# Kernel optimization log

Hardware: AMD Instinct MI355X
Metric: run time of the kernel (lower is better)

## Reference

```python
import jax, jax.numpy as jnp
import numpy as np

IN_FEATURES = 4096
OUT_FEATURES = 4096
N_TOKENS = 1024

@jax.custom_vjp
def binarize(w):
    # UnipolarSte.forward: (w > 0).float()
    return (w > 0).astype(w.dtype)

def _bin_fwd(w):
    return binarize(w), None

def _bin_bwd(_, g):
    # UnipolarSte.backward: F.hardtanh(grad_output) == clip(g, -1, 1)
    return (jnp.clip(g, -1.0, 1.0),)

binarize.defvjp(_bin_fwd, _bin_bwd)

def setup_inputs() -> dict:
    key = jax.random.key(0)
    kx, kw = jax.random.split(key)
    x = jax.random.normal(kx, (N_TOKENS, IN_FEATURES), dtype=jnp.float32)
    weight = jax.random.normal(kw, (OUT_FEATURES, IN_FEATURES), dtype=jnp.float32)
    scaling_factor = jnp.ones((OUT_FEATURES,), dtype=jnp.float32)
    return {"x": x, "weight": weight, "scaling_factor": scaling_factor}

def reference(x, weight, scaling_factor):
    w_b = binarize(weight)                      # [out, in] in {0,1}
    out = jnp.einsum('ni,oi->no', x, w_b)       # F.linear(x, w_b)
    # s_eff = round(clamp(s,1)).detach() - s.detach() + s
    s_round = jax.lax.stop_gradient(jnp.round(jnp.clip(scaling_factor, 1.0, None)))
    s_eff = s_round - jax.lax.stop_gradient(scaling_factor) + scaling_factor
    return out * s_eff[None, :]
```

## Files before the change

### kernel.cpp

```cpp
#include <hip/hip_runtime.h>

#define M_TOK 1024
#define NOUT  4096
#define KIN   4096
#define KBYTES (KIN / 8)

#define BM 128
#define BN 128
#define BK 64
#define NKT (KIN / BK)

typedef __attribute__((ext_vector_type(8))) short bf16x8_t;
typedef __attribute__((ext_vector_type(4))) float f32x4_t;

__global__ __launch_bounds__(256) void prep_w(const float* __restrict__ w,
                                              unsigned long long* __restrict__ wbits) {
  const int lane = threadIdx.x & 63;
  const int row  = blockIdx.x * 4 + (threadIdx.x >> 6);
  const float* wr = w + (size_t)row * KIN;
  unsigned long long mine = 0;
#pragma unroll 16
  for (int q = 0; q < 64; ++q) {
    float v = wr[q * 64 + lane];
    unsigned long long m = __ballot(v > 0.f);
    if (lane == q) mine = m;
  }
  wbits[(size_t)row * 64 + lane] = mine;
}

__device__ __forceinline__ unsigned pack_bf16(float a, float b) {
  unsigned ua = __float_as_uint(a);
  unsigned ub = __float_as_uint(b);
  ua = (ua + 0x7FFFu + ((ua >> 16) & 1u)) >> 16;
  ub = (ub + 0x7FFFu + ((ub >> 16) & 1u)) >> 16;
  return ua | (ub << 16);
}

__global__ __launch_bounds__(256) void prep_x(const float4* __restrict__ x4,
                                              uint2* __restrict__ xb) {
  const size_t t = blockIdx.x * 256 + threadIdx.x;
  float4 v = x4[t];
  xb[t] = make_uint2(pack_bf16(v.x, v.y), pack_bf16(v.z, v.w));
}

__global__ __launch_bounds__(512, 2) void gemm_bin_kernel(
    const unsigned short* __restrict__ A,
    const unsigned char* __restrict__ Wb,
    const float* __restrict__ sf,
    float* __restrict__ C) {
  __shared__ __align__(16) unsigned short As[2][BM * BK];
  __shared__ __align__(16) unsigned short Bs[2][BN * BK];

  const int tid  = threadIdx.x;
  const int lane = tid & 63;
  const int wave = tid >> 6;
  const int wm   = (wave >> 2) * 64;
  const int wn   = (wave & 3) * 32;
  const int quad = lane >> 4;
  const int l16  = lane & 15;
  const int m0   = blockIdx.y * BM;
  const int n0   = blockIdx.x * BN;

  const int r  = tid >> 2;
  const int j2 = tid & 3;
  const unsigned short* gA = A + (size_t)(m0 + r) * KIN + j2 * 16;
  const unsigned char*  gB = Wb + (size_t)(n0 + r) * KBYTES + j2 * 2;
  const int cw0 = ((2 * j2 + 0 + r) & 7);
  const int cw1 = ((2 * j2 + 1 + r) & 7);
  const int woA0 = r * BK + cw0 * 8, woA1 = r * BK + cw1 * 8;

  f32x4_t acc[4][2];
#pragma unroll
  for (int i = 0; i < 4; ++i)
#pragma unroll
    for (int j = 0; j < 2; ++j)
      acc[i][j] = (f32x4_t){0.f, 0.f, 0.f, 0.f};

  uint4 sa0 = *(const uint4*)gA;
  uint4 sa1 = *(const uint4*)(gA + 8);
  unsigned short sb = *(const unsigned short*)gB;

  for (int kt = 0; kt < NKT; ++kt) {
    const int cur = kt & 1;
    uint4 bx0, bx1;
    bx0.x = (sb & 0x1u    ? 0x3F80u : 0u) | (sb & 0x2u    ? 0x3F800000u : 0u);
    bx0.y = (sb & 0x4u    ? 0x3F80u : 0u) | (sb & 0x8u    ? 0x3F800000u : 0u);
    bx0.z = (sb & 0x10u   ? 0x3F80u : 0u) | (sb & 0x20u   ? 0x3F800000u : 0u);
    bx0.w = (sb & 0x40u   ? 0x3F80u : 0u) | (sb & 0x80u   ? 0x3F800000u : 0u);
    bx1.x = (sb & 0x100u  ? 0x3F80u : 0u) | (sb & 0x200u  ? 0x3F800000u : 0u);
    bx1.y = (sb & 0x400u  ? 0x3F80u : 0u) | (sb & 0x800u  ? 0x3F800000u : 0u);
    bx1.z = (sb & 0x1000u ? 0x3F80u : 0u) | (sb & 0x2000u ? 0x3F800000u : 0u);
    bx1.w = (sb & 0x4000u ? 0x3F80u : 0u) | (sb & 0x8000u ? 0x3F800000u : 0u);
    *(uint4*)&As[cur][woA0] = sa0;
    *(uint4*)&As[cur][woA1] = sa1;
    *(uint4*)&Bs[cur][woA0] = bx0;
    *(uint4*)&Bs[cur][woA1] = bx1;
    __syncthreads();
    if (kt + 1 < NKT) {
      const int off = (kt + 1) * BK;
      sa0 = *(const uint4*)(gA + off);
      sa1 = *(const uint4*)(gA + off + 8);
      sb  = *(const unsigned short*)(gB + (kt + 1) * 8);
    }
    bf16x8_t af[2][4], bfr[2][2];
#pragma unroll
    for (int ks = 0; ks < 2; ++ks) {
#pragma unroll
      for (int i = 0; i < 4; ++i) {
        const int ra = wm + i * 16 + l16;
        af[ks][i] = *(const bf16x8_t*)&As[cur][ra * BK + ((ks * 4 + quad + ra) & 7) * 8];
      }
#pragma unroll
      for (int j = 0; j < 2; ++j) {
        const int rb = wn + j * 16 + l16;
        bfr[ks][j] = *(const bf16x8_t*)&Bs[cur][rb * BK + ((ks * 4 + quad + rb) & 7) * 8];
      }
    }
#pragma unroll
    for (int ks = 0; ks < 2; ++ks)
#pragma unroll
      for (int i = 0; i < 4; ++i)
#pragma unroll
        for (int j = 0; j < 2; ++j)
          acc[i][j] = __builtin_amdgcn_mfma_f32_16x16x32_bf16(af[ks][i], bfr[ks][j],
                                                              acc[i][j], 0, 0, 0);
  }

#pragma unroll
  for (int j = 0; j < 2; ++j) {
    const int n = n0 + wn + j * 16 + l16;
    const float s = rintf(fmaxf(sf[n], 1.0f));
#pragma unroll
    for (int i = 0; i < 4; ++i) {
      const int mr = m0 + wm + i * 16 + quad * 4;
#pragma unroll
      for (int rr = 0; rr < 4; ++rr)
        C[(size_t)(mr + rr) * NOUT + n] = acc[i][j][rr] * s;
    }
  }
}

extern "C" void kernel_launch(void* const* d_in, const int* in_sizes, int n_in,
                              void* d_out, int out_size, void* d_ws, size_t ws_size,
                              hipStream_t stream) {
  const float* x  = (const float*)d_in[0];
  const float* w  = (const float*)d_in[1];
  const float* sf = (const float*)d_in[2];
  float* out = (float*)d_out;

  unsigned char*  Wbits = (unsigned char*)d_ws;
  unsigned short* Xb    = (unsigned short*)((char*)d_ws + (1u << 21));

  prep_w<<<1024, 256, 0, stream>>>(w, (unsigned long long*)Wbits);
  prep_x<<<4096, 256, 0, stream>>>((const float4*)x, (uint2*)Xb);

  dim3 grid(NOUT / BN, M_TOK / BM);
  gemm_bin_kernel<<<grid, 512, 0, stream>>>(Xb, Wbits, sf, out);
}
```

Baseline: 171.7 us.

## Prepack X and weight bits into MFMA fragment order and drop LDS staging

Adds a second weight prep pass that reorders the bit-packed weights into per-lane MFMA fragment order, and makes the X prep write bf16 directly in fragment layout. The GEMM then loads operands straight from global memory into registers with a two-stage register double buffer. This removes shared memory, barriers and the LDS round trip. Tiles become 128x64 per block with 4 waves. The cost is an extra prep launch, and each wave rereads A fragments from global/L2 with no LDS sharing across waves.

```diff
diff --git a/kernel.cpp b/kernel.cpp
--- a/kernel.cpp
+++ b/kernel.cpp
@@ -3,15 +3,10 @@
 #define M_TOK 1024
 #define NOUT  4096
 #define KIN   4096
-#define KBYTES (KIN / 8)
-
-#define BM 128
-#define BN 128
-#define BK 64
-#define NKT (KIN / BK)
 
 typedef __attribute__((ext_vector_type(8))) short bf16x8_t;
 typedef __attribute__((ext_vector_type(4))) float f32x4_t;
+
 
 __global__ __launch_bounds__(256) void prep_w(const float* __restrict__ w,
                                               unsigned long long* __restrict__ wbits) {
@@ -28,6 +23,17 @@
   wbits[(size_t)row * 64 + lane] = mine;
 }
 
+__global__ __launch_bounds__(256) void prep_w2(const unsigned long long* __restrict__ wbits,
+                                               unsigned short* __restrict__ bfrag) {
+  const unsigned t = blockIdx.x * 256 + threadIdx.x;
+  const int l = t & 63, kt = (t >> 6) & 63, n16 = t >> 12;
+  const int row = n16 * 16 + (l & 15), quad = l >> 4;
+  unsigned long long w64 = wbits[(size_t)row * 64 + kt];
+  unsigned b0 = (unsigned)(w64 >> (quad * 8)) & 0xFFu;
+  unsigned b1 = (unsigned)(w64 >> (quad * 8 + 32)) & 0xFFu;
+  bfrag[t] = (unsigned short)(b0 | (b1 << 8));
+}
+
 __device__ __forceinline__ unsigned pack_bf16(float a, float b) {
   unsigned ua = __float_as_uint(a);
   unsigned ub = __float_as_uint(b);
@@ -37,37 +43,41 @@
 }
 
 __global__ __launch_bounds__(256) void prep_x(const float4* __restrict__ x4,
-                                              uint2* __restrict__ xb) {
-  const size_t t = blockIdx.x * 256 + threadIdx.x;
-  float4 v = x4[t];
-  xb[t] = make_uint2(pack_bf16(v.x, v.y), pack_bf16(v.z, v.w));
+                                              uint4* __restrict__ xfrag) {
+  const unsigned t = blockIdx.x * 256 + threadIdx.x;
+  const int l = t & 63;
+  const unsigned f = t >> 6;
+  const int m16 = f >> 7, k32 = f & 127;
+  const int row = m16 * 16 + (l & 15);
+  const int c4  = k32 * 8 + (l >> 4) * 2;
+  const float4* p = x4 + (size_t)row * (KIN / 4) + c4;
+  float4 a = p[0], b = p[1];
+  uint4 o;
+  o.x = pack_bf16(a.x, a.y);
+  o.y = pack_bf16(a.z, a.w);
+  o.z = pack_bf16(b.x, b.y);
+  o.w = pack_bf16(b.z, b.w);
+  xfrag[t] = o;
 }
 
-__global__ __launch_bounds__(512, 2) void gemm_bin_kernel(
-    const unsigned short* __restrict__ A,
-    const unsigned char* __restrict__ Wb,
+__global__ __launch_bounds__(256, 2) void gemm_bin_kernel(
+    const unsigned short* __restrict__ Xf,
+    const unsigned short* __restrict__ Bf,
     const float* __restrict__ sf,
     float* __restrict__ C) {
-  __shared__ __align__(16) unsigned short As[2][BM * BK];
-  __shared__ __align__(16) unsigned short Bs[2][BN * BK];
-
   const int tid  = threadIdx.x;
   const int lane = tid & 63;
   const int wave = tid >> 6;
-  const int wm   = (wave >> 2) * 64;
-  const int wn   = (wave & 3) * 32;
   const int quad = lane >> 4;
   const int l16  = lane & 15;
-  const int m0   = blockIdx.y * BM;
-  const int n0   = blockIdx.x * BN;
+  const unsigned bid = blockIdx.x;
+  const int by = bid & 7, bx = bid >> 3;
+  const int m0 = by * 128, n0 = bx * 64;
+  const int wm = (wave >> 1) * 64, wn = (wave & 1) * 32;
+  const int m16b = (m0 + wm) >> 4;
+  const int n16b = (n0 + wn) >> 4;
 
-  const int r  = tid >> 2;
-  const int j2 = tid & 3;
-  const unsigned short* gA = A + (size_t)(m0 + r) * KIN + j2 * 16;
-  const unsigned char*  gB = Wb + (size_t)(n0 + r) * KBYTES + j2 * 2;
-  const int cw0 = ((2 * j2 + 0 + r) & 7);
-  const int cw1 = ((2 * j2 + 1 + r) & 7);
-  const int woA0 = r * BK + cw0 * 8, woA1 = r * BK + cw1 * 8;
+  const uint4* Xf4 = (const uint4*)Xf;
 
   f32x4_t acc[4][2];
 #pragma unroll
@@ -76,54 +86,46 @@
     for (int j = 0; j < 2; ++j)
       acc[i][j] = (f32x4_t){0.f, 0.f, 0.f, 0.f};
 
-  uint4 sa0 = *(const uint4*)gA;
-  uint4 sa1 = *(const uint4*)(gA + 8);
-  unsigned short sb = *(const unsigned short*)gB;
+  auto load_kt = [&](uint4 (&ar)[4][2], unsigned (&br)[2], int kt) {
+#pragma unroll
+    for (int i = 0; i < 4; ++i)
+#pragma unroll
+      for (int ks = 0; ks < 2; ++ks)
+        ar[i][ks] = Xf4[((size_t)(m16b + i) * 128 + kt * 2 + ks) * 64 + lane];
+#pragma unroll
+    for (int j = 0; j < 2; ++j)
+      br[j] = Bf[((n16b + j) * 64 + kt) * 64 + lane];
+  };
 
-  for (int kt = 0; kt < NKT; ++kt) {
-    const int cur = kt & 1;
-    uint4 bx0, bx1;
-    bx0.x = (sb & 0x1u    ? 0x3F80u : 0u) | (sb & 0x2u    ? 0x3F800000u : 0u);
-    bx0.y = (sb & 0x4u    ? 0x3F80u : 0u) | (sb & 0x8u    ? 0x3F800000u : 0u);
-    bx0.z = (sb & 0x10u   ? 0x3F80u : 0u) | (sb & 0x20u   ? 0x3F800000u : 0u);
-    bx0.w = (sb & 0x40u   ? 0x3F80u : 0u) | (sb & 0x80u   ? 0x3F800000u : 0u);
-    bx1.x = (sb & 0x100u  ? 0x3F80u : 0u) | (sb & 0x200u  ? 0x3F800000u : 0u);
-    bx1.y = (sb & 0x400u  ? 0x3F80u : 0u) | (sb & 0x800u  ? 0x3F800000u : 0u);
-    bx1.z = (sb & 0x1000u ? 0x3F80u : 0u) | (sb & 0x2000u ? 0x3F800000u : 0u);
-    bx1.w = (sb & 0x4000u ? 0x3F80u : 0u) | (sb & 0x8000u ? 0x3F800000u : 0u);
-    *(uint4*)&As[cur][woA0] = sa0;
-    *(uint4*)&As[cur][woA1] = sa1;
-    *(uint4*)&Bs[cur][woA0] = bx0;
-    *(uint4*)&Bs[cur][woA1] = bx1;
-    __syncthreads();
-    if (kt + 1 < NKT) {
-      const int off = (kt + 1) * BK;
-      sa0 = *(const uint4*)(gA + off);
-      sa1 = *(const uint4*)(gA + off + 8);
-      sb  = *(const unsigned short*)(gB + (kt + 1) * 8);
-    }
-    bf16x8_t af[2][4], bfr[2][2];
+  auto compute = [&](uint4 (&ar)[4][2], unsigned (&br)[2]) {
 #pragma unroll
-    for (int ks = 0; ks < 2; ++ks) {
+    for (int j = 0; j < 2; ++j)
 #pragma unroll
-      for (int i = 0; i < 4; ++i) {
-        const int ra = wm + i * 16 + l16;
-        af[ks][i] = *(const bf16x8_t*)&As[cur][ra * BK + ((ks * 4 + quad + ra) & 7) * 8];
+      for (int ks = 0; ks < 2; ++ks) {
+        unsigned byte = (br[j] >> (ks * 8)) & 0xFFu;
+        union { unsigned u[4]; bf16x8_t v; } ex;
+#pragma unroll
+        for (int p = 0; p < 4; ++p) {
+          unsigned tt = (byte >> (2 * p)) & 3u;
+          ex.u[p] = ((tt | (tt << 15)) & 0x10001u) * 0x3F80u;
+        }
+#pragma unroll
+        for (int i = 0; i < 4; ++i) {
+          union { uint4 q; bf16x8_t v; } av;
+          av.q = ar[i][ks];
+          acc[i][j] = __builtin_amdgcn_mfma_f32_16x16x32_bf16(av.v, ex.v, acc[i][j], 0, 0, 0);
+        }
       }
-#pragma unroll
-      for (int j = 0; j < 2; ++j) {
-        const int rb = wn + j * 16 + l16;
-        bfr[ks][j] = *(const bf16x8_t*)&Bs[cur][rb * BK + ((ks * 4 + quad + rb) & 7) * 8];
-      }
-    }
-#pragma unroll
-    for (int ks = 0; ks < 2; ++ks)
-#pragma unroll
-      for (int i = 0; i < 4; ++i)
-#pragma unroll
-        for (int j = 0; j < 2; ++j)
-          acc[i][j] = __builtin_amdgcn_mfma_f32_16x16x32_bf16(af[ks][i], bfr[ks][j],
-                                                              acc[i][j], 0, 0, 0);
+  };
+
+  uint4 aA[4][2], aB[4][2];
+  unsigned bA[2], bB[2];
+  load_kt(aA, bA, 0);
+  for (int kt = 0; kt < 64; kt += 2) {
+    load_kt(aB, bB, kt + 1);
+    compute(aA, bA);
+    if (kt + 2 < 64) load_kt(aA, bA, kt + 2);
+    compute(aB, bB);
   }
 
 #pragma unroll
@@ -134,8 +136,8 @@
     for (int i = 0; i < 4; ++i) {
       const int mr = m0 + wm + i * 16 + quad * 4;
 #pragma unroll
-      for (int rr = 0; rr < 4; ++rr)
-        C[(size_t)(mr + rr) * NOUT + n] = acc[i][j][rr] * s;
+      for (int r = 0; r < 4; ++r)
+        C[(size_t)(mr + r) * NOUT + n] = acc[i][j][r] * s;
     }
   }
 }
@@ -148,12 +150,13 @@
   const float* sf = (const float*)d_in[2];
   float* out = (float*)d_out;
 
-  unsigned char*  Wbits = (unsigned char*)d_ws;
-  unsigned short* Xb    = (unsigned short*)((char*)d_ws + (1u << 21));
+  unsigned short*     Bfrag = (unsigned short*)d_ws;
+  unsigned long long* Wbits = (unsigned long long*)((char*)d_ws + (2u << 20));
+  unsigned short*     Xfrag = (unsigned short*)((char*)d_ws + (4u << 20));
 
-  prep_w<<<1024, 256, 0, stream>>>(w, (unsigned long long*)Wbits);
-  prep_x<<<4096, 256, 0, stream>>>((const float4*)x, (uint2*)Xb);
+  prep_w<<<1024, 256, 0, stream>>>(w, Wbits);
+  prep_w2<<<4096, 256, 0, stream>>>(Wbits, Bfrag);
+  prep_x<<<2048, 256, 0, stream>>>((const float4*)x, (uint4*)Xfrag);
 
-  dim3 grid(NOUT / BN, M_TOK / BM);
-  gemm_bin_kernel<<<grid, 512, 0, stream>>>(Xb, Wbits, sf, out);
+  gemm_bin_kernel<<<512, 256, 0, stream>>>(Xfrag, Bfrag, sf, out);
 }
```

New measurement: 154.4 us. 10.1% less time.
